# Optimization experiments

Measured on AMD Instinct MI355X. Metric: run time of the kernel, lower is better.

## Reference

```python
import jax, jax.numpy as jnp
import numpy as np

N_NODES = 50000
N_EDGES = 600000
IN_DIM = 128
FEAT = 128
N_CLS = 40


def _lin_params(key, fan_in, fan_out, bias=True):
    k1, k2 = jax.random.split(key)
    lim = 1.0 / np.sqrt(fan_in)
    W = jax.random.uniform(k1, (fan_out, fan_in), jnp.float32, -lim, lim)
    b = jax.random.uniform(k2, (fan_out,), jnp.float32, -lim, lim) if bias else None
    return W, b


def setup_inputs() -> dict:
    key = jax.random.key(0)
    ks = jax.random.split(key, 8)
    x = jax.random.normal(ks[0], (N_NODES, IN_DIM), jnp.float32)
    edge_index = jax.random.randint(ks[1], (2, N_EDGES), 0, N_NODES, jnp.int64 if jax.config.read('jax_enable_x64') else jnp.int32)
    Wl1, bl1 = _lin_params(ks[2], IN_DIM, FEAT)
    Wr1, _ = _lin_params(ks[3], IN_DIM, FEAT, bias=False)
    Wl2, bl2 = _lin_params(ks[4], FEAT, FEAT)
    Wr2, _ = _lin_params(ks[5], FEAT, FEAT, bias=False)
    Wl3, bl3 = _lin_params(ks[6], FEAT, FEAT)
    Wr3, _ = _lin_params(ks[7], FEAT, FEAT, bias=False)
    kc = jax.random.fold_in(key, 99)
    Wc, bc = _lin_params(kc, FEAT, N_CLS)
    return {"x": x, "edge_index": edge_index,
            "Wl1": Wl1, "bl1": bl1, "Wr1": Wr1,
            "Wl2": Wl2, "bl2": bl2, "Wr2": Wr2,
            "Wl3": Wl3, "bl3": bl3, "Wr3": Wr3,
            "Wc": Wc, "bc": bc}


def _sage_relu(x, src, dst, deg_inv, Wl, bl, Wr):
    # mean aggregation over incoming neighbors: gather at src, scatter-add at dst
    agg = jax.ops.segment_sum(x[src], dst, num_segments=N_NODES)  # [N, F]
    agg = agg * deg_inv[:, None]
    out = agg @ Wl.T + bl + x @ Wr.T  # W1*mean(neigh) + W2*x_root
    return jax.nn.relu(out)


def reference(x, edge_index, Wl1, bl1, Wr1, Wl2, bl2, Wr2, Wl3, bl3, Wr3, Wc, bc):
    src, dst = edge_index[0], edge_index[1]
    deg = jax.ops.segment_sum(jnp.ones((src.shape[0],), x.dtype), dst, num_segments=N_NODES)
    deg_inv = 1.0 / jnp.maximum(deg, 1.0)
    local_repr = _sage_relu(x, src, dst, deg_inv, Wl1, bl1, Wr1)
    global_repr = _sage_relu(local_repr, src, dst, deg_inv, Wl2, bl2, Wr2)
    # invariant_feature_extractor: one SAGEConvwithRelu + (eval-mode) dropout + residual
    h = _sage_relu(global_repr, src, dst, deg_inv, Wl3, bl3, Wr3)
    vanilla_if = h + global_repr
    vanilla_pred = vanilla_if @ Wc.T + bc
    return vanilla_pred
```

## Files before the change

kernel.cpp:

```cpp
#include <hip/hip_runtime.h>
#include <hip/hip_bf16.h>

constexpr int N_NODES = 50000;
constexpr int N_EDGES = 600000;
constexpr int D       = 128;
constexpr int N_CLS   = 40;

using bf16x8 = __attribute__((ext_vector_type(8))) short;
using f32x4  = __attribute__((ext_vector_type(4))) float;

__device__ inline unsigned short f2bf(float f) {
    __hip_bfloat16 h = __float2bfloat16(f);
    return __builtin_bit_cast(unsigned short, h);
}
__device__ inline float bf2f(unsigned short u) {
    __hip_bfloat16 h = __builtin_bit_cast(__hip_bfloat16, u);
    return __bfloat162float(h);
}


__global__ void hist_kernel(const int* __restrict__ ei, int* __restrict__ cnt) {
    int e = blockIdx.x * 256 + threadIdx.x;
    if (e < N_EDGES) atomicAdd(&cnt[ei[N_EDGES + e]], 1);
}

__global__ __launch_bounds__(1024) void scan_block_kernel(const int* __restrict__ cnt,
                                                          int* __restrict__ rs,
                                                          int* __restrict__ bsum, int n) {
    __shared__ int t[1024];
    int tid = threadIdx.x;
    int gid = blockIdx.x * 1024 + tid;
    int v = (gid < n) ? cnt[gid] : 0;
    t[tid] = v;
    __syncthreads();
    for (int off = 1; off < 1024; off <<= 1) {
        int u = (tid >= off) ? t[tid - off] : 0;
        __syncthreads();
        t[tid] += u;
        __syncthreads();
    }
    if (gid < n) rs[gid] = t[tid] - v;
    if (tid == 1023) bsum[blockIdx.x] = t[1023];
}

__global__ void scan_sums_kernel(const int* __restrict__ bsum, int* __restrict__ boff, int nblk) {
    __shared__ int t[64];
    int tid = threadIdx.x;
    int v = (tid < nblk) ? bsum[tid] : 0;
    t[tid] = v;
    __syncthreads();
    for (int off = 1; off < 64; off <<= 1) {
        int u = (tid >= off) ? t[tid - off] : 0;
        __syncthreads();
        t[tid] += u;
        __syncthreads();
    }
    if (tid < nblk) boff[tid] = t[tid] - v;
}

__global__ void finalize_kernel(const int* __restrict__ cnt, int* __restrict__ rs,
                                int* __restrict__ cursor, float* __restrict__ dinv,
                                const int* __restrict__ boff) {
    int i = blockIdx.x * 256 + threadIdx.x;
    if (i < N_NODES) {
        int v = rs[i] + boff[i >> 10];
        rs[i] = v;
        cursor[i] = v;
        dinv[i] = 1.0f / fmaxf((float)cnt[i], 1.0f);
        if (i == 0) rs[N_NODES] = N_EDGES;
    }
}

__global__ void scatter_kernel(const int* __restrict__ ei, int* __restrict__ cursor,
                               int* __restrict__ csr) {
    int e = blockIdx.x * 256 + threadIdx.x;
    if (e < N_EDGES) {
        int d = ei[N_EDGES + e];
        int p = atomicAdd(&cursor[d], 1);
        csr[p] = ei[e];
    }
}

__global__ void split_w_kernel(const float* __restrict__ Wl, const float* __restrict__ Wr,
                               unsigned short* __restrict__ hi, unsigned short* __restrict__ lo) {
    int idx = blockIdx.x * 256 + threadIdx.x;
    int n = idx >> 8, k = idx & 255;
    float v = (k < 128) ? Wl[n * 128 + k] : Wr[n * 128 + (k - 128)];
    unsigned short h = f2bf(v);
    hi[idx] = h;
    lo[idx] = f2bf(v - bf2f(h));
}

__global__ __launch_bounds__(256) void agg_kernel(const float* __restrict__ feat,
                                                  const int* __restrict__ rs,
                                                  const int* __restrict__ csr,
                                                  const float* __restrict__ dinv,
                                                  float* __restrict__ aggn) {
    int wave = threadIdx.x >> 6;
    int lane = threadIdx.x & 63;
    int node = blockIdx.x * 4 + wave;
    if (node >= N_NODES) return;
    int e0 = rs[node], e1 = rs[node + 1];
    int half = lane >> 5;
    int fl = lane & 31;
    float ax = 0.f, ay = 0.f, az = 0.f, aw = 0.f;

    for (int base = e0; base < e1; base += 64) {
        int cnt = min(64, e1 - base);
        int idxv = (lane < cnt) ? csr[base + lane] : 0;
        int cnt2 = cnt & ~1;
        int j = 0;
        for (; j + 8 <= cnt2; j += 8) {
            int s0 = __shfl(idxv, j + half);
            int s1 = __shfl(idxv, j + 2 + half);
            int s2 = __shfl(idxv, j + 4 + half);
            int s3 = __shfl(idxv, j + 6 + half);
            float4 v0 = *(const float4*)&feat[(size_t)s0 * D + fl * 4];
            float4 v1 = *(const float4*)&feat[(size_t)s1 * D + fl * 4];
            float4 v2 = *(const float4*)&feat[(size_t)s2 * D + fl * 4];
            float4 v3 = *(const float4*)&feat[(size_t)s3 * D + fl * 4];
            ax += v0.x + v1.x + v2.x + v3.x;
            ay += v0.y + v1.y + v2.y + v3.y;
            az += v0.z + v1.z + v2.z + v3.z;
            aw += v0.w + v1.w + v2.w + v3.w;
        }
        for (; j < cnt2; j += 2) {
            int s = __shfl(idxv, j + half);
            float4 v = *(const float4*)&feat[(size_t)s * D + fl * 4];
            ax += v.x; ay += v.y; az += v.z; aw += v.w;
        }
        if (j < cnt) {
            int s = __shfl(idxv, j);
            if (half == 0) {
                float4 v = *(const float4*)&feat[(size_t)s * D + fl * 4];
                ax += v.x; ay += v.y; az += v.z; aw += v.w;
            }
        }
    }
    ax += __shfl(ax, lane ^ 32);
    ay += __shfl(ay, lane ^ 32);
    az += __shfl(az, lane ^ 32);
    aw += __shfl(aw, lane ^ 32);
    if (half == 0) {
        float di = dinv[node];
        float4 o; o.x = ax * di; o.y = ay * di; o.z = az * di; o.w = aw * di;
        *(float4*)&aggn[(size_t)node * D + fl * 4] = o;
    }
}

__global__ __launch_bounds__(256) void gemm_mfma_kernel(const float* __restrict__ Aagg,
                                                        const float* __restrict__ Ax,
                                                        const unsigned short* __restrict__ Whi,
                                                        const unsigned short* __restrict__ Wlo,
                                                        const float* __restrict__ bias,
                                                        const float* __restrict__ resid,
                                                        float* __restrict__ outp, int M) {
    __shared__ __align__(16) unsigned short AhS[64 * 64];
    __shared__ __align__(16) unsigned short AlS[64 * 64];
    __shared__ __align__(16) unsigned short WhS[128 * 64];
    __shared__ __align__(16) unsigned short WlS[128 * 64];
    char* AhB = (char*)AhS;
    char* AlB = (char*)AlS;
    char* WhB = (char*)WhS;
    char* WlB = (char*)WlS;

    int tid = threadIdx.x;
    int lane = tid & 63;
    int wid = tid >> 6;
    int wr = wid >> 1;
    int wc = wid & 1;
    int lr = lane & 15;
    int kg = (lane >> 4) * 8;
    int row0 = blockIdx.x * 64;

    f32x4 acc[2][4];
#pragma unroll
    for (int f = 0; f < 2; ++f)
#pragma unroll
        for (int j = 0; j < 4; ++j) acc[f][j] = (f32x4){0.f, 0.f, 0.f, 0.f};

    for (int kt = 0; kt < 4; ++kt) {
        const float* Asrc = (kt < 2) ? Aagg : Ax;
        int kcol = (kt & 1) * 64;

#pragma unroll
        for (int it = 0; it < 2; ++it) {
            int slot = tid + it * 256;
            int row = slot >> 3;
            int k8 = (slot & 7) * 8;
            int gr = row0 + row;
            if (gr >= M) gr = M - 1;
            const float* p = &Asrc[(size_t)gr * D + kcol + k8];
            float4 v0 = *(const float4*)p;
            float4 v1 = *(const float4*)(p + 4);
            float fv[8] = {v0.x, v0.y, v0.z, v0.w, v1.x, v1.y, v1.z, v1.w};
            union { unsigned short u[8]; uint4 q; } ph, pl;
#pragma unroll
            for (int j = 0; j < 8; ++j) {
                unsigned short h = f2bf(fv[j]);
                ph.u[j] = h;
                pl.u[j] = f2bf(fv[j] - bf2f(h));
            }
            int boff = (row << 7) + (k8 << 1);
            boff ^= (row & 7) << 4;
            *(uint4*)(AhB + boff) = ph.q;
            *(uint4*)(AlB + boff) = pl.q;
        }
#pragma unroll
        for (int it = 0; it < 4; ++it) {
            int slot = tid + it * 256;
            int n = slot >> 3;
            int k8 = (slot & 7) * 8;
            size_t gsrc = (size_t)n * 256 + kt * 64 + k8;
            uint4 h = *(const uint4*)&Whi[gsrc];
            uint4 l = *(const uint4*)&Wlo[gsrc];
            int boff = (n << 7) + (k8 << 1);
            boff ^= (n & 7) << 4;
            *(uint4*)(WhB + boff) = h;
            *(uint4*)(WlB + boff) = l;
        }
        __syncthreads();

#pragma unroll
        for (int ks = 0; ks < 2; ++ks) {
            int kk = ks * 32 + kg;
            bf16x8 ah[2], al[2];
#pragma unroll
            for (int f = 0; f < 2; ++f) {
                int row = wr * 32 + f * 16 + lr;
                int boff = (row << 7) + (kk << 1);
                boff ^= (row & 7) << 4;
                ah[f] = *(const bf16x8*)(AhB + boff);
                al[f] = *(const bf16x8*)(AlB + boff);
            }
            bf16x8 bh[4], bl[4];
#pragma unroll
            for (int j = 0; j < 4; ++j) {
                int n = wc * 64 + j * 16 + lr;
                int boff = (n << 7) + (kk << 1);
                boff ^= (n & 7) << 4;
                bh[j] = *(const bf16x8*)(WhB + boff);
                bl[j] = *(const bf16x8*)(WlB + boff);
            }
#pragma unroll
            for (int f = 0; f < 2; ++f)
#pragma unroll
                for (int j = 0; j < 4; ++j) {
                    acc[f][j] = __builtin_amdgcn_mfma_f32_16x16x32_bf16(ah[f], bh[j], acc[f][j], 0, 0, 0);
                    acc[f][j] = __builtin_amdgcn_mfma_f32_16x16x32_bf16(ah[f], bl[j], acc[f][j], 0, 0, 0);
                    acc[f][j] = __builtin_amdgcn_mfma_f32_16x16x32_bf16(al[f], bh[j], acc[f][j], 0, 0, 0);
                }
        }
        __syncthreads();
    }

#pragma unroll
    for (int f = 0; f < 2; ++f)
#pragma unroll
        for (int j = 0; j < 4; ++j) {
            int c = wc * 64 + j * 16 + lr;
            float b = bias[c];
#pragma unroll
            for (int r = 0; r < 4; ++r) {
                int gr = row0 + wr * 32 + f * 16 + (lane >> 4) * 4 + r;
                if (gr < M) {
                    float v = acc[f][j][r] + b;
                    v = fmaxf(v, 0.f);
                    if (resid) v += resid[(size_t)gr * D + c];
                    outp[(size_t)gr * D + c] = v;
                }
            }
        }
}

__global__ __launch_bounds__(256) void classifier_kernel(const float* __restrict__ vif,
                                                         const float* __restrict__ Wc,
                                                         const float* __restrict__ bc,
                                                         float* __restrict__ outp, int M) {
    __shared__ float Vs[64][D + 4];
    __shared__ float Cs[N_CLS][D + 4];
    int tid = threadIdx.x;
    int row0 = blockIdx.x * 64;

#pragma unroll
    for (int l = 0; l < 8; ++l) {
        int slot = tid + l * 256;
        int r = slot >> 5;
        int kq = slot & 31;
        int gr = row0 + r;
        if (gr >= M) gr = M - 1;
        float4 v = *(const float4*)&vif[(size_t)gr * D + kq * 4];
        *(float4*)&Vs[r][kq * 4] = v;
    }
#pragma unroll
    for (int l = 0; l < 5; ++l) {
        int slot = tid + l * 256;
        int r = slot >> 5;
        int kq = slot & 31;
        float4 v = *(const float4*)&Wc[r * D + kq * 4];
        *(float4*)&Cs[r][kq * 4] = v;
    }
    __syncthreads();

    int r2 = tid >> 3;
    int cg = tid & 7;
    float acc[2][5] = {};
#pragma unroll 4
    for (int k4 = 0; k4 < 32; ++k4) {
        float4 a0 = *(const float4*)&Vs[r2 * 2][k4 * 4];
        float4 a1 = *(const float4*)&Vs[r2 * 2 + 1][k4 * 4];
#pragma unroll
        for (int j = 0; j < 5; ++j) {
            float4 w = *(const float4*)&Cs[cg * 5 + j][k4 * 4];
            acc[0][j] = fmaf(a0.x, w.x, fmaf(a0.y, w.y, fmaf(a0.z, w.z, fmaf(a0.w, w.w, acc[0][j]))));
            acc[1][j] = fmaf(a1.x, w.x, fmaf(a1.y, w.y, fmaf(a1.z, w.z, fmaf(a1.w, w.w, acc[1][j]))));
        }
    }
#pragma unroll
    for (int i = 0; i < 2; ++i) {
        int r = row0 + r2 * 2 + i;
        if (r >= M) continue;
#pragma unroll
        for (int j = 0; j < 5; ++j) {
            int c = cg * 5 + j;
            outp[(size_t)r * N_CLS + c] = acc[i][j] + bc[c];
        }
    }
}

extern "C" void kernel_launch(void* const* d_in, const int* in_sizes, int n_in,
                              void* d_out, int out_size, void* d_ws, size_t ws_size,
                              hipStream_t stream) {
    const float* x   = (const float*)d_in[0];
    const int*   ei  = (const int*)d_in[1];
    const float* Wl1 = (const float*)d_in[2];
    const float* bl1 = (const float*)d_in[3];
    const float* Wr1 = (const float*)d_in[4];
    const float* Wl2 = (const float*)d_in[5];
    const float* bl2 = (const float*)d_in[6];
    const float* Wr2 = (const float*)d_in[7];
    const float* Wl3 = (const float*)d_in[8];
    const float* bl3 = (const float*)d_in[9];
    const float* Wr3 = (const float*)d_in[10];
    const float* Wc  = (const float*)d_in[11];
    const float* bc  = (const float*)d_in[12];
    float* out = (float*)d_out;

    char* w = (char*)d_ws;
    size_t off = 0;
    auto carve = [&](size_t bytes) -> void* {
        void* p = w + off;
        off = (off + bytes + 255) & ~(size_t)255;
        return p;
    };
    int*   cnt    = (int*)carve((size_t)N_NODES * 4);
    int*   rs     = (int*)carve((size_t)(N_NODES + 1) * 4);
    int*   cursor = (int*)carve((size_t)N_NODES * 4);
    float* dinv   = (float*)carve((size_t)N_NODES * 4);
    int*   bsum   = (int*)carve(64 * 4);
    int*   boff   = (int*)carve(64 * 4);
    int*   csr    = (int*)carve((size_t)N_EDGES * 4);
    float* aggn   = (float*)carve((size_t)N_NODES * D * 4);
    float* bufA   = (float*)carve((size_t)N_NODES * D * 4);
    float* bufB   = (float*)carve((size_t)N_NODES * D * 4);
    unsigned short* w1h = (unsigned short*)carve(128 * 256 * 2);
    unsigned short* w1l = (unsigned short*)carve(128 * 256 * 2);
    unsigned short* w2h = (unsigned short*)carve(128 * 256 * 2);
    unsigned short* w2l = (unsigned short*)carve(128 * 256 * 2);
    unsigned short* w3h = (unsigned short*)carve(128 * 256 * 2);
    unsigned short* w3l = (unsigned short*)carve(128 * 256 * 2);
    (void)ws_size;

    const int NBLK_SCAN = (N_NODES + 1023) / 1024;
    const int GRID_E = (N_EDGES + 255) / 256;
    const int GRID_N = (N_NODES + 255) / 256;
    const int GRID_AGG = (N_NODES + 3) / 4;
    const int GRID_GEMM = (N_NODES + 63) / 64;

    hipMemsetAsync(cnt, 0, (size_t)N_NODES * 4, stream);
    hipLaunchKernelGGL(hist_kernel, dim3(GRID_E), dim3(256), 0, stream, ei, cnt);
    hipLaunchKernelGGL(split_w_kernel, dim3(128), dim3(256), 0, stream, Wl1, Wr1, w1h, w1l);
    hipLaunchKernelGGL(split_w_kernel, dim3(128), dim3(256), 0, stream, Wl2, Wr2, w2h, w2l);
    hipLaunchKernelGGL(split_w_kernel, dim3(128), dim3(256), 0, stream, Wl3, Wr3, w3h, w3l);
    hipLaunchKernelGGL(scan_block_kernel, dim3(NBLK_SCAN), dim3(1024), 0, stream, cnt, rs, bsum, N_NODES);
    hipLaunchKernelGGL(scan_sums_kernel, dim3(1), dim3(64), 0, stream, bsum, boff, NBLK_SCAN);
    hipLaunchKernelGGL(finalize_kernel, dim3(GRID_N), dim3(256), 0, stream, cnt, rs, cursor, dinv, boff);
    hipLaunchKernelGGL(scatter_kernel, dim3(GRID_E), dim3(256), 0, stream, ei, cursor, csr);

    hipLaunchKernelGGL(agg_kernel, dim3(GRID_AGG), dim3(256), 0, stream, x, rs, csr, dinv, aggn);
    hipLaunchKernelGGL(gemm_mfma_kernel, dim3(GRID_GEMM), dim3(256), 0, stream,
                       aggn, x, w1h, w1l, bl1, (const float*)nullptr, bufA, N_NODES);
    hipLaunchKernelGGL(agg_kernel, dim3(GRID_AGG), dim3(256), 0, stream, bufA, rs, csr, dinv, aggn);
    hipLaunchKernelGGL(gemm_mfma_kernel, dim3(GRID_GEMM), dim3(256), 0, stream,
                       aggn, bufA, w2h, w2l, bl2, (const float*)nullptr, bufB, N_NODES);
    hipLaunchKernelGGL(agg_kernel, dim3(GRID_AGG), dim3(256), 0, stream, bufB, rs, csr, dinv, aggn);
    hipLaunchKernelGGL(gemm_mfma_kernel, dim3(GRID_GEMM), dim3(256), 0, stream,
                       aggn, bufB, w3h, w3l, bl3, bufB, bufA, N_NODES);
    hipLaunchKernelGGL(classifier_kernel, dim3(GRID_GEMM), dim3(256), 0, stream,
                       bufA, Wc, bc, out, N_NODES);
}
```

Baseline: 385.5 us.

## Fuse final SAGE layer GEMM with classifier and batch weight splitting

The third layer's GEMM now keeps its ReLU+residual output in shared memory as split bf16 hi/lo and immediately runs the 128->40 classifier with MFMA. This removes the write and re-read of the 50000x128 intermediate and one launch. The three per-layer weight split launches are also merged into one, plus a padded classifier weight split. The classifier moves from fp32 FMA to three-pass bf16 MFMA, which may shift numerics slightly. The fused kernel uses 48 KB of shared memory, which may lower occupancy.

```diff
diff --git a/kernel.cpp b/kernel.cpp
--- a/kernel.cpp
+++ b/kernel.cpp
@@ -81,11 +81,27 @@
     }
 }
 
-__global__ void split_w_kernel(const float* __restrict__ Wl, const float* __restrict__ Wr,
-                               unsigned short* __restrict__ hi, unsigned short* __restrict__ lo) {
+__global__ void split_w3_kernel(const float* __restrict__ Wl1, const float* __restrict__ Wr1,
+                                const float* __restrict__ Wl2, const float* __restrict__ Wr2,
+                                const float* __restrict__ Wl3, const float* __restrict__ Wr3,
+                                unsigned short* __restrict__ hi, unsigned short* __restrict__ lo) {
+    int layer = blockIdx.x >> 7;
+    int idx = (blockIdx.x & 127) * 256 + threadIdx.x;
+    int n = idx >> 8, k = idx & 255;
+    const float* Wl = (layer == 0) ? Wl1 : (layer == 1) ? Wl2 : Wl3;
+    const float* Wr = (layer == 0) ? Wr1 : (layer == 1) ? Wr2 : Wr3;
+    float v = (k < 128) ? Wl[n * 128 + k] : Wr[n * 128 + (k - 128)];
+    unsigned short h = f2bf(v);
+    size_t o = (size_t)layer * 32768 + idx;
+    hi[o] = h;
+    lo[o] = f2bf(v - bf2f(h));
+}
+
+__global__ void split_wc_kernel(const float* __restrict__ Wc,
+                                unsigned short* __restrict__ hi, unsigned short* __restrict__ lo) {
     int idx = blockIdx.x * 256 + threadIdx.x;
-    int n = idx >> 8, k = idx & 255;
-    float v = (k < 128) ? Wl[n * 128 + k] : Wr[n * 128 + (k - 128)];
+    int n = idx >> 7, k = idx & 127;
+    float v = (n < N_CLS) ? Wc[n * 128 + k] : 0.f;
     unsigned short h = f2bf(v);
     hi[idx] = h;
     lo[idx] = f2bf(v - bf2f(h));
@@ -153,7 +169,6 @@
                                                         const unsigned short* __restrict__ Whi,
                                                         const unsigned short* __restrict__ Wlo,
                                                         const float* __restrict__ bias,
-                                                        const float* __restrict__ resid,
                                                         float* __restrict__ outp, int M) {
     __shared__ __align__(16) unsigned short AhS[64 * 64];
     __shared__ __align__(16) unsigned short AlS[64 * 64];
@@ -264,66 +279,195 @@
             for (int r = 0; r < 4; ++r) {
                 int gr = row0 + wr * 32 + f * 16 + (lane >> 4) * 4 + r;
                 if (gr < M) {
-                    float v = acc[f][j][r] + b;
-                    v = fmaxf(v, 0.f);
-                    if (resid) v += resid[(size_t)gr * D + c];
+                    float v = fmaxf(acc[f][j][r] + b, 0.f);
                     outp[(size_t)gr * D + c] = v;
                 }
             }
         }
 }
 
-__global__ __launch_bounds__(256) void classifier_kernel(const float* __restrict__ vif,
-                                                         const float* __restrict__ Wc,
-                                                         const float* __restrict__ bc,
-                                                         float* __restrict__ outp, int M) {
-    __shared__ float Vs[64][D + 4];
-    __shared__ float Cs[N_CLS][D + 4];
+__global__ __launch_bounds__(256) void gemm_cls_kernel(const float* __restrict__ Aagg,
+                                                       const float* __restrict__ Ax,
+                                                       const unsigned short* __restrict__ Whi,
+                                                       const unsigned short* __restrict__ Wlo,
+                                                       const float* __restrict__ bias,
+                                                       const float* __restrict__ residf,
+                                                       const unsigned short* __restrict__ Wch,
+                                                       const unsigned short* __restrict__ Wcl,
+                                                       const float* __restrict__ bc,
+                                                       float* __restrict__ outp, int M) {
+    __shared__ __align__(16) char smem[49152];
+    char* AhB = smem;
+    char* AlB = smem + 8192;
+    char* WhB = smem + 16384;
+    char* WlB = smem + 32768;
+
     int tid = threadIdx.x;
+    int lane = tid & 63;
+    int wid = tid >> 6;
+    int wr = wid >> 1;
+    int wc = wid & 1;
+    int lr = lane & 15;
+    int kg = (lane >> 4) * 8;
     int row0 = blockIdx.x * 64;
 
-#pragma unroll
-    for (int l = 0; l < 8; ++l) {
-        int slot = tid + l * 256;
-        int r = slot >> 5;
-        int kq = slot & 31;
-        int gr = row0 + r;
-        if (gr >= M) gr = M - 1;
-        float4 v = *(const float4*)&vif[(size_t)gr * D + kq * 4];
-        *(float4*)&Vs[r][kq * 4] = v;
-    }
-#pragma unroll
-    for (int l = 0; l < 5; ++l) {
-        int slot = tid + l * 256;
-        int r = slot >> 5;
-        int kq = slot & 31;
-        float4 v = *(const float4*)&Wc[r * D + kq * 4];
-        *(float4*)&Cs[r][kq * 4] = v;
-    }
-    __syncthreads();
-
-    int r2 = tid >> 3;
-    int cg = tid & 7;
-    float acc[2][5] = {};
-#pragma unroll 4
-    for (int k4 = 0; k4 < 32; ++k4) {
-        float4 a0 = *(const float4*)&Vs[r2 * 2][k4 * 4];
-        float4 a1 = *(const float4*)&Vs[r2 * 2 + 1][k4 * 4];
-#pragma unroll
-        for (int j = 0; j < 5; ++j) {
-            float4 w = *(const float4*)&Cs[cg * 5 + j][k4 * 4];
-            acc[0][j] = fmaf(a0.x, w.x, fmaf(a0.y, w.y, fmaf(a0.z, w.z, fmaf(a0.w, w.w, acc[0][j]))));
-            acc[1][j] = fmaf(a1.x, w.x, fmaf(a1.y, w.y, fmaf(a1.z, w.z, fmaf(a1.w, w.w, acc[1][j]))));
-        }
-    }
-#pragma unroll
-    for (int i = 0; i < 2; ++i) {
-        int r = row0 + r2 * 2 + i;
-        if (r >= M) continue;
-#pragma unroll
-        for (int j = 0; j < 5; ++j) {
-            int c = cg * 5 + j;
-            outp[(size_t)r * N_CLS + c] = acc[i][j] + bc[c];
+    f32x4 acc[2][4];
+#pragma unroll
+    for (int f = 0; f < 2; ++f)
+#pragma unroll
+        for (int j = 0; j < 4; ++j) acc[f][j] = (f32x4){0.f, 0.f, 0.f, 0.f};
+
+    for (int kt = 0; kt < 4; ++kt) {
+        const float* Asrc = (kt < 2) ? Aagg : Ax;
+        int kcol = (kt & 1) * 64;
+#pragma unroll
+        for (int it = 0; it < 2; ++it) {
+            int slot = tid + it * 256;
+            int row = slot >> 3;
+            int k8 = (slot & 7) * 8;
+            int gr = row0 + row;
+            if (gr >= M) gr = M - 1;
+            const float* p = &Asrc[(size_t)gr * D + kcol + k8];
+            float4 v0 = *(const float4*)p;
+            float4 v1 = *(const float4*)(p + 4);
+            float fv[8] = {v0.x, v0.y, v0.z, v0.w, v1.x, v1.y, v1.z, v1.w};
+            union { unsigned short u[8]; uint4 q; } ph, pl;
+#pragma unroll
+            for (int j = 0; j < 8; ++j) {
+                unsigned short h = f2bf(fv[j]);
+                ph.u[j] = h;
+                pl.u[j] = f2bf(fv[j] - bf2f(h));
+            }
+            int boff = (row << 7) + (k8 << 1);
+            boff ^= (row & 7) << 4;
+            *(uint4*)(AhB + boff) = ph.q;
+            *(uint4*)(AlB + boff) = pl.q;
+        }
+#pragma unroll
+        for (int it = 0; it < 4; ++it) {
+            int slot = tid + it * 256;
+            int n = slot >> 3;
+            int k8 = (slot & 7) * 8;
+            size_t gsrc = (size_t)n * 256 + kt * 64 + k8;
+            uint4 h = *(const uint4*)&Whi[gsrc];
+            uint4 l = *(const uint4*)&Wlo[gsrc];
+            int boff = (n << 7) + (k8 << 1);
+            boff ^= (n & 7) << 4;
+            *(uint4*)(WhB + boff) = h;
+            *(uint4*)(WlB + boff) = l;
+        }
+        __syncthreads();
+#pragma unroll
+        for (int ks = 0; ks < 2; ++ks) {
+            int kk = ks * 32 + kg;
+            bf16x8 ah[2], al[2];
+#pragma unroll
+            for (int f = 0; f < 2; ++f) {
+                int row = wr * 32 + f * 16 + lr;
+                int boff = (row << 7) + (kk << 1);
+                boff ^= (row & 7) << 4;
+                ah[f] = *(const bf16x8*)(AhB + boff);
+                al[f] = *(const bf16x8*)(AlB + boff);
+            }
+            bf16x8 bh[4], bl[4];
+#pragma unroll
+            for (int j = 0; j < 4; ++j) {
+                int n = wc * 64 + j * 16 + lr;
+                int boff = (n << 7) + (kk << 1);
+                boff ^= (n & 7) << 4;
+                bh[j] = *(const bf16x8*)(WhB + boff);
+                bl[j] = *(const bf16x8*)(WlB + boff);
+            }
+#pragma unroll
+            for (int f = 0; f < 2; ++f)
+#pragma unroll
+                for (int j = 0; j < 4; ++j) {
+                    acc[f][j] = __builtin_amdgcn_mfma_f32_16x16x32_bf16(ah[f], bh[j], acc[f][j], 0, 0, 0);
+                    acc[f][j] = __builtin_amdgcn_mfma_f32_16x16x32_bf16(ah[f], bl[j], acc[f][j], 0, 0, 0);
+                    acc[f][j] = __builtin_amdgcn_mfma_f32_16x16x32_bf16(al[f], bh[j], acc[f][j], 0, 0, 0);
+                }
+        }
+        __syncthreads();
+    }
+
+    f32x4 acc2[3];
+#pragma unroll
+    for (int j = 0; j < 3; ++j) acc2[j] = (f32x4){0.f, 0.f, 0.f, 0.f};
+
+    for (int p = 0; p < 2; ++p) {
+#pragma unroll
+        for (int it = 0; it < 2; ++it) {
+            int slot = tid + it * 256;
+            if (slot < 384) {
+                int n = slot >> 3;
+                int k8 = (slot & 7) * 8;
+                size_t gsrc = (size_t)n * 128 + p * 64 + k8;
+                uint4 h = *(const uint4*)&Wch[gsrc];
+                uint4 l = *(const uint4*)&Wcl[gsrc];
+                int boff = (n << 7) + (k8 << 1);
+                boff ^= (n & 7) << 4;
+                *(uint4*)(WhB + boff) = h;
+                *(uint4*)(WlB + boff) = l;
+            }
+        }
+        if (wc == p) {
+#pragma unroll
+            for (int f = 0; f < 2; ++f)
+#pragma unroll
+                for (int j = 0; j < 4; ++j) {
+                    int c = wc * 64 + j * 16 + lr;
+                    float b = bias[c];
+#pragma unroll
+                    for (int r = 0; r < 4; ++r) {
+                        int row = wr * 32 + f * 16 + (lane >> 4) * 4 + r;
+                        int gr = row0 + row;
+                        int gra = (gr < M) ? gr : (M - 1);
+                        float v = fmaxf(acc[f][j][r] + b, 0.f);
+                        v += residf[(size_t)gra * D + c];
+                        int kloc = j * 16 + lr;
+                        int boff = (row << 7) + (kloc << 1);
+                        boff ^= (row & 7) << 4;
+                        unsigned short h = f2bf(v);
+                        *(unsigned short*)(AhB + boff) = h;
+                        *(unsigned short*)(AlB + boff) = f2bf(v - bf2f(h));
+                    }
+                }
+        }
+        __syncthreads();
+
+#pragma unroll
+        for (int ks = 0; ks < 2; ++ks) {
+            int kk = ks * 32 + kg;
+            int row = wid * 16 + lr;
+            int boffA = (row << 7) + (kk << 1);
+            boffA ^= (row & 7) << 4;
+            bf16x8 ah = *(const bf16x8*)(AhB + boffA);
+            bf16x8 al = *(const bf16x8*)(AlB + boffA);
+#pragma unroll
+            for (int j = 0; j < 3; ++j) {
+                int n = j * 16 + lr;
+                int boffB = (n << 7) + (kk << 1);
+                boffB ^= (n & 7) << 4;
+                bf16x8 bh = *(const bf16x8*)(WhB + boffB);
+                bf16x8 bl = *(const bf16x8*)(WlB + boffB);
+                acc2[j] = __builtin_amdgcn_mfma_f32_16x16x32_bf16(ah, bh, acc2[j], 0, 0, 0);
+                acc2[j] = __builtin_amdgcn_mfma_f32_16x16x32_bf16(ah, bl, acc2[j], 0, 0, 0);
+                acc2[j] = __builtin_amdgcn_mfma_f32_16x16x32_bf16(al, bh, acc2[j], 0, 0, 0);
+            }
+        }
+        __syncthreads();
+    }
+
+#pragma unroll
+    for (int j = 0; j < 3; ++j) {
+        int c = j * 16 + lr;
+        if (c < N_CLS) {
+            float b = bc[c];
+#pragma unroll
+            for (int r = 0; r < 4; ++r) {
+                int gr = row0 + wid * 16 + (lane >> 4) * 4 + r;
+                if (gr < M) outp[(size_t)gr * N_CLS + c] = acc2[j][r] + b;
+            }
         }
     }
 }
@@ -363,12 +507,10 @@
     float* aggn   = (float*)carve((size_t)N_NODES * D * 4);
     float* bufA   = (float*)carve((size_t)N_NODES * D * 4);
     float* bufB   = (float*)carve((size_t)N_NODES * D * 4);
-    unsigned short* w1h = (unsigned short*)carve(128 * 256 * 2);
-    unsigned short* w1l = (unsigned short*)carve(128 * 256 * 2);
-    unsigned short* w2h = (unsigned short*)carve(128 * 256 * 2);
-    unsigned short* w2l = (unsigned short*)carve(128 * 256 * 2);
-    unsigned short* w3h = (unsigned short*)carve(128 * 256 * 2);
-    unsigned short* w3l = (unsigned short*)carve(128 * 256 * 2);
+    unsigned short* w123h = (unsigned short*)carve(3 * 128 * 256 * 2);
+    unsigned short* w123l = (unsigned short*)carve(3 * 128 * 256 * 2);
+    unsigned short* wch   = (unsigned short*)carve(48 * 128 * 2);
+    unsigned short* wcl   = (unsigned short*)carve(48 * 128 * 2);
     (void)ws_size;
 
     const int NBLK_SCAN = (N_NODES + 1023) / 1024;
@@ -379,9 +521,9 @@
 
     hipMemsetAsync(cnt, 0, (size_t)N_NODES * 4, stream);
     hipLaunchKernelGGL(hist_kernel, dim3(GRID_E), dim3(256), 0, stream, ei, cnt);
-    hipLaunchKernelGGL(split_w_kernel, dim3(128), dim3(256), 0, stream, Wl1, Wr1, w1h, w1l);
-    hipLaunchKernelGGL(split_w_kernel, dim3(128), dim3(256), 0, stream, Wl2, Wr2, w2h, w2l);
-    hipLaunchKernelGGL(split_w_kernel, dim3(128), dim3(256), 0, stream, Wl3, Wr3, w3h, w3l);
+    hipLaunchKernelGGL(split_w3_kernel, dim3(384), dim3(256), 0, stream,
+                       Wl1, Wr1, Wl2, Wr2, Wl3, Wr3, w123h, w123l);
+    hipLaunchKernelGGL(split_wc_kernel, dim3(24), dim3(256), 0, stream, Wc, wch, wcl);
     hipLaunchKernelGGL(scan_block_kernel, dim3(NBLK_SCAN), dim3(1024), 0, stream, cnt, rs, bsum, N_NODES);
     hipLaunchKernelGGL(scan_sums_kernel, dim3(1), dim3(64), 0, stream, bsum, boff, NBLK_SCAN);
     hipLaunchKernelGGL(finalize_kernel, dim3(GRID_N), dim3(256), 0, stream, cnt, rs, cursor, dinv, boff);
@@ -389,13 +531,12 @@
 
     hipLaunchKernelGGL(agg_kernel, dim3(GRID_AGG), dim3(256), 0, stream, x, rs, csr, dinv, aggn);
     hipLaunchKernelGGL(gemm_mfma_kernel, dim3(GRID_GEMM), dim3(256), 0, stream,
-                       aggn, x, w1h, w1l, bl1, (const float*)nullptr, bufA, N_NODES);
+                       aggn, x, w123h, w123l, bl1, bufA, N_NODES);
     hipLaunchKernelGGL(agg_kernel, dim3(GRID_AGG), dim3(256), 0, stream, bufA, rs, csr, dinv, aggn);
     hipLaunchKernelGGL(gemm_mfma_kernel, dim3(GRID_GEMM), dim3(256), 0, stream,
-                       aggn, bufA, w2h, w2l, bl2, (const float*)nullptr, bufB, N_NODES);
+                       aggn, bufA, w123h + 32768, w123l + 32768, bl2, bufB, N_NODES);
     hipLaunchKernelGGL(agg_kernel, dim3(GRID_AGG), dim3(256), 0, stream, bufB, rs, csr, dinv, aggn);
-    hipLaunchKernelGGL(gemm_mfma_kernel, dim3(GRID_GEMM), dim3(256), 0, stream,
-                       aggn, bufB, w3h, w3l, bl3, bufB, bufA, N_NODES);
-    hipLaunchKernelGGL(classifier_kernel, dim3(GRID_GEMM), dim3(256), 0, stream,
-                       bufA, Wc, bc, out, N_NODES);
-}
+    hipLaunchKernelGGL(gemm_cls_kernel, dim3(GRID_GEMM), dim3(256), 0, stream,
+                       aggn, bufB, w123h + 65536, w123l + 65536, bl3, bufB,
+                       wch, wcl, bc, out, N_NODES);
+}
```

Result: faster. 360.7 us (-6.4%).
